# Performance work log

Measured on AMD Instinct MI355X. Metric: run time of the kernel, lower is better.

Reference implementation:

```python
import jax, jax.numpy as jnp
import numpy as np

LN_EPS = 1e-5

def _conv1d_same(x, w, b):
    # x: [B, L, Cin], w: [K, Cin, Cout] (kernel=3, padding=1 -> SAME)
    y = jax.lax.conv_general_dilated(x, w, window_strides=(1,), padding=[(1, 1)],
                                     dimension_numbers=('NWC', 'WIO', 'NWC'))
    return y + b

def _layer_norm(x, g, b):
    mu = jnp.mean(x, axis=-1, keepdims=True)
    var = jnp.var(x, axis=-1, keepdims=True)
    return (x - mu) * jax.lax.rsqrt(var + LN_EPS) * g + b

def _duration_predictor(x, conv1_w, conv1_b, ln1_g, ln1_b, conv2_w, conv2_b, ln2_g, ln2_b, lin_w, lin_b):
    h = jax.nn.relu(_layer_norm(_conv1d_same(x, conv1_w, conv1_b), ln1_g, ln1_b))
    h = jax.nn.relu(_layer_norm(_conv1d_same(h, conv2_w, conv2_b), ln2_g, ln2_b))
    out = jax.nn.relu(h @ lin_w + lin_b)  # [B, L, 1]
    return out[..., 0]  # squeeze -> [B, L]

def _length_regulate(x, dur, T):
    # Equivalent of alignment @ x without materializing [B, T, L] one-hot matrix.
    # Frame t copies phoneme j where cumsum(dur)[j-1] <= t < cumsum(dur)[j].
    ends = jnp.cumsum(dur, axis=-1)          # [B, L]
    total = ends[:, -1]                       # [B]
    t = jnp.arange(T)
    idx = jax.vmap(lambda e: jnp.searchsorted(e, t, side='right'))(ends)  # [B, T]
    idx = jnp.minimum(idx, dur.shape[1] - 1)
    gathered = jnp.take_along_axis(x, idx[:, :, None], axis=1)            # [B, T, D]
    mask = t[None, :] < total[:, None]                                    # [B, T]
    return jnp.where(mask[:, :, None], gathered, 0.0)

def setup_inputs() -> dict:
    key = jax.random.key(0)
    ks = jax.random.split(key, 8)
    B, L, D, F = 64, 512, 256, 256
    inp = {
        'x': jax.random.normal(ks[0], (B, L, D), dtype=jnp.float32),
        'target': jax.random.randint(ks[1], (B, L), 0, 8, dtype=jnp.int32),
        'mel_max_length': 4096,
        'conv1_w': jax.random.normal(ks[2], (3, D, F), dtype=jnp.float32) * 0.05,
        'conv1_b': jnp.zeros((F,), jnp.float32),
        'ln1_g': jnp.ones((F,), jnp.float32),
        'ln1_b': jnp.zeros((F,), jnp.float32),
        'conv2_w': jax.random.normal(ks[3], (3, F, F), dtype=jnp.float32) * 0.05,
        'conv2_b': jnp.zeros((F,), jnp.float32),
        'ln2_g': jnp.ones((F,), jnp.float32),
        'ln2_b': jnp.zeros((F,), jnp.float32),
        'lin_w': jax.random.normal(ks[4], (F, 1), dtype=jnp.float32) * 0.05,
        'lin_b': jnp.zeros((1,), jnp.float32),
    }
    return inp

def reference(x, target, mel_max_length, conv1_w, conv1_b, ln1_g, ln1_b, conv2_w, conv2_b, ln2_g, ln2_b, lin_w, lin_b):
    # Training path of LengthRegulator.forward (target given, dropout eval-mode identity)
    dp_out = _duration_predictor(x, conv1_w, conv1_b, ln1_g, ln1_b, conv2_w, conv2_b, ln2_g, ln2_b, lin_w, lin_b)
    output = _length_regulate(x, target, mel_max_length)  # padded to mel_max_length
    return output, dp_out
```

## Files before the change

kernel.cpp:

```cpp
#include <hip/hip_runtime.h>

#define B 64
#define L 512
#define D 256
#define T 4096
#define LN_EPS 1e-5f

typedef __attribute__((ext_vector_type(8))) short bf16x8;
typedef __attribute__((ext_vector_type(4))) float f32x4;

__device__ __forceinline__ unsigned short f2bf(float f) {
    unsigned int u = __float_as_uint(f);
    unsigned int r = (u + 0x7FFFu + ((u >> 16) & 1u)) >> 16;
    return (unsigned short)r;
}

__global__ __launch_bounds__(256) void cvt_w_kernel(const float* __restrict__ w1,
                                                    const float* __restrict__ w2,
                                                    unsigned short* __restrict__ o1,
                                                    unsigned short* __restrict__ o2) {
    const float* in = blockIdx.y ? w2 : w1;
    unsigned short* out = blockIdx.y ? o2 : o1;
    const int k = blockIdx.x;
    const int d0 = blockIdx.z * 32;
    const int f = threadIdx.x;
    for (int dc = 0; dc < 32; dc += 8) {
        unsigned short v[8];
#pragma unroll
        for (int i = 0; i < 8; ++i) v[i] = f2bf(in[(k * 256 + d0 + dc + i) * 256 + f]);
        *(bf16x8*)(out + (k * 256 + f) * 256 + d0 + dc) = *(bf16x8*)v;
    }
}

__global__ __launch_bounds__(64) void cumsum_kernel(const int* __restrict__ target,
                                                    int* __restrict__ ends) {
    int b = blockIdx.x;
    int lane = threadIdx.x;
    const int* trow = target + b * L;
    int* erow = ends + b * L;
    int vals[8];
    int base = lane * 8;
#pragma unroll
    for (int j = 0; j < 8; ++j) vals[j] = trow[base + j];
#pragma unroll
    for (int j = 1; j < 8; ++j) vals[j] += vals[j - 1];
    int lsum = vals[7];
    int s = lsum;
#pragma unroll
    for (int off = 1; off < 64; off <<= 1) {
        int v = __shfl_up(s, off, 64);
        if (lane >= off) s += v;
    }
    int excl = s - lsum;
#pragma unroll
    for (int j = 0; j < 8; ++j) erow[base + j] = excl + vals[j];
}

template <bool IN_F32, bool FUSE_LINEAR>
__global__ __launch_bounds__(256, 2) void conv_fused_kernel(
    const void* __restrict__ xin,
    const unsigned short* __restrict__ wT,
    const float* __restrict__ bias, const float* __restrict__ g, const float* __restrict__ beta,
    const float* __restrict__ lin_w, const float* __restrict__ lin_b,
    unsigned short* __restrict__ hout,
    float* __restrict__ dp)
{
    constexpr int LS = 264;
    __shared__ __align__(16) unsigned short xs[66 * LS];
    __shared__ float psum[64][2];
    __shared__ float psq[64][2];
    __shared__ float muA[64], rsA[64];

    const int tid = threadIdx.x;
    const int lane = tid & 63;
    const int wid = tid >> 6;
    const int l15 = lane & 15;
    const int g4 = lane >> 4;
    const int b = blockIdx.y;
    const int l0 = blockIdx.x * 64;
    const int wm = (wid >> 1) * 32;
    const int wn = (wid & 1) * 128;

    for (int i = tid; i < 66 * 32; i += 256) {
        int r = i >> 5, c = i & 31;
        int grow = l0 - 1 + r;
        bf16x8 v = {0, 0, 0, 0, 0, 0, 0, 0};
        if (grow >= 0 && grow < L) {
            if constexpr (IN_F32) {
                const float* xr = (const float*)xin + ((size_t)(b * L + grow)) * D + c * 8;
                float4 f0 = *(const float4*)xr;
                float4 f1 = *(const float4*)(xr + 4);
                unsigned short t[8] = {f2bf(f0.x), f2bf(f0.y), f2bf(f0.z), f2bf(f0.w),
                                       f2bf(f1.x), f2bf(f1.y), f2bf(f1.z), f2bf(f1.w)};
                v = *(bf16x8*)t;
            } else {
                v = *(const bf16x8*)((const unsigned short*)xin + ((size_t)(b * L + grow)) * D + c * 8);
            }
        }
        *(bf16x8*)(xs + r * LS + c * 8) = v;
    }
    __syncthreads();

    f32x4 acc[2][8];
#pragma unroll
    for (int m = 0; m < 2; ++m)
#pragma unroll
        for (int n = 0; n < 8; ++n) acc[m][n] = (f32x4){0.f, 0.f, 0.f, 0.f};

#pragma unroll 4
    for (int ks = 0; ks < 24; ++ks) {
        const int tap = ks >> 3, kk = ks & 7;
        const int r0 = wm + l15 + tap;
        bf16x8 a0 = *(const bf16x8*)(xs + r0 * LS + kk * 32 + g4 * 8);
        bf16x8 a1 = *(const bf16x8*)(xs + (r0 + 16) * LS + kk * 32 + g4 * 8);
        const unsigned short* wp = wT + tap * 65536 + (wn + l15) * 256 + kk * 32 + g4 * 8;
#pragma unroll
        for (int n = 0; n < 8; ++n) {
            bf16x8 bf = *(const bf16x8*)(wp + n * 4096);
            acc[0][n] = __builtin_amdgcn_mfma_f32_16x16x32_bf16(a0, bf, acc[0][n], 0, 0, 0);
            acc[1][n] = __builtin_amdgcn_mfma_f32_16x16x32_bf16(a1, bf, acc[1][n], 0, 0, 0);
        }
    }

    float biasv[8], gv[8], bv[8], lwv[8];
#pragma unroll
    for (int n = 0; n < 8; ++n) {
        int col = wn + n * 16 + l15;
        biasv[n] = bias[col];
        gv[n] = g[col];
        bv[n] = beta[col];
        lwv[n] = FUSE_LINEAR ? lin_w[col] : 0.f;
    }

#pragma unroll
    for (int m = 0; m < 2; ++m)
#pragma unroll
        for (int j = 0; j < 4; ++j) {
            float s = 0.f, q = 0.f;
#pragma unroll
            for (int n = 0; n < 8; ++n) {
                float v = acc[m][n][j] + biasv[n];
                s += v;
                q += v * v;
            }
#pragma unroll
            for (int off = 1; off < 16; off <<= 1) {
                s += __shfl_xor(s, off, 64);
                q += __shfl_xor(q, off, 64);
            }
            if (l15 == 0) {
                int row = wm + m * 16 + g4 * 4 + j;
                psum[row][wid & 1] = s;
                psq[row][wid & 1] = q;
            }
        }
    __syncthreads();
    if (tid < 64) {
        float s = psum[tid][0] + psum[tid][1];
        float q = psq[tid][0] + psq[tid][1];
        float mu = s * (1.f / 256.f);
        float var = q * (1.f / 256.f) - mu * mu;
        muA[tid] = mu;
        rsA[tid] = rsqrtf(var + LN_EPS);
    }
    __syncthreads();

    if constexpr (!FUSE_LINEAR) {
#pragma unroll
        for (int m = 0; m < 2; ++m)
#pragma unroll
            for (int j = 0; j < 4; ++j) {
                int row = wm + m * 16 + g4 * 4 + j;
                float mu = muA[row], rs = rsA[row];
                size_t base = ((size_t)(b * L + l0 + row)) * D + wn + l15;
#pragma unroll
                for (int n = 0; n < 8; ++n) {
                    float v = acc[m][n][j] + biasv[n];
                    float y = fmaxf((v - mu) * rs * gv[n] + bv[n], 0.f);
                    hout[base + n * 16] = f2bf(y);
                }
            }
    } else {
        float lb0 = lin_b[0];
#pragma unroll
        for (int m = 0; m < 2; ++m)
#pragma unroll
            for (int j = 0; j < 4; ++j) {
                int row = wm + m * 16 + g4 * 4 + j;
                float mu = muA[row], rs = rsA[row];
                float p = 0.f;
#pragma unroll
                for (int n = 0; n < 8; ++n) {
                    float v = acc[m][n][j] + biasv[n];
                    float y = fmaxf((v - mu) * rs * gv[n] + bv[n], 0.f);
                    p += y * lwv[n];
                }
#pragma unroll
                for (int off = 1; off < 16; off <<= 1) p += __shfl_xor(p, off, 64);
                if (l15 == 0) psum[row][wid & 1] = p;
            }
        __syncthreads();
        if (tid < 64) dp[b * L + l0 + tid] = fmaxf(psum[tid][0] + psum[tid][1] + lb0, 0.f);
    }
}

__global__ __launch_bounds__(256) void length_regulate_kernel(
    const float* __restrict__ x, const int* __restrict__ ends, float* __restrict__ out) {
    __shared__ int sidx[256];
    const int tid = threadIdx.x;
    const int lane = tid & 63;
    const int wid = tid >> 6;
    const int b = blockIdx.y;
    const int t0 = blockIdx.x * 256;
    const int* e = ends + b * L;
    const int total = e[L - 1];
    {
        int t = t0 + tid;
        int lo = 0, hi = L;
        while (lo < hi) {
            int mid = (lo + hi) >> 1;
            if (e[mid] <= t) lo = mid + 1; else hi = mid;
        }
        sidx[tid] = (lo < L - 1) ? lo : (L - 1);
    }
    __syncthreads();
    const float4* x4 = (const float4*)(x + (size_t)b * L * D);
    float4* o4 = (float4*)(out + (size_t)b * T * D);
    const float4 z = make_float4(0.f, 0.f, 0.f, 0.f);
#pragma unroll 4
    for (int rr = 0; rr < 64; ++rr) {
        int row = wid * 64 + rr;
        int t = t0 + row;
        float4 v = z;
        if (t < total) v = x4[sidx[row] * 64 + lane];
        o4[t * 64 + lane] = v;
    }
}

extern "C" void kernel_launch(void* const* d_in, const int* in_sizes, int n_in,
                              void* d_out, int out_size, void* d_ws, size_t ws_size,
                              hipStream_t stream) {
    const float* x   = (const float*)d_in[0];
    const int* target = (const int*)d_in[1];
    const float* c1w = (const float*)d_in[3];
    const float* c1b = (const float*)d_in[4];
    const float* g1  = (const float*)d_in[5];
    const float* b1  = (const float*)d_in[6];
    const float* c2w = (const float*)d_in[7];
    const float* c2b = (const float*)d_in[8];
    const float* g2  = (const float*)d_in[9];
    const float* b2  = (const float*)d_in[10];
    const float* lw  = (const float*)d_in[11];
    const float* lb  = (const float*)d_in[12];

    float* out = (float*)d_out;
    float* dp  = out + (size_t)B * T * D;

    char* base = (char*)d_out;
    unsigned short* h1  = (unsigned short*)(base);
    unsigned short* wT1 = (unsigned short*)(base + (32u << 20));
    unsigned short* wT2 = (unsigned short*)(base + (32u << 20) + 393216);
    int* ends = (int*)d_ws;

    cvt_w_kernel<<<dim3(3, 2, 8), dim3(256), 0, stream>>>(c1w, c2w, wT1, wT2);
    cumsum_kernel<<<dim3(B), dim3(64), 0, stream>>>(target, ends);
    conv_fused_kernel<true, false><<<dim3(L / 64, B), dim3(256), 0, stream>>>(
        x, wT1, c1b, g1, b1, nullptr, nullptr, h1, nullptr);
    conv_fused_kernel<false, true><<<dim3(L / 64, B), dim3(256), 0, stream>>>(
        h1, wT2, c2b, g2, b2, lw, lb, nullptr, dp);
    length_regulate_kernel<<<dim3(T / 256, B), dim3(256), 0, stream>>>(x, ends, out);
}
```

Baseline: 445.5 us.

## Merge prep kernels, halve conv row tile with weight prefetch, smem ends and nontemporal stores

The weight-conversion and cumsum kernels are merged into one launch. The conv kernel now uses 32-row tiles with one 16-row MFMA strip per wave, software-prefetches the next k-step's weight fragments into registers, and raises its occupancy hint to 3 blocks per CU. The length-regulate kernel stages the cumsum row in shared memory for its binary search and writes the large output with nontemporal stores. Smaller tiles double the number of conv blocks and halve reuse of each weight load per block, which raises global or L2 weight traffic.

```diff
diff --git a/kernel.cpp b/kernel.cpp
--- a/kernel.cpp
+++ b/kernel.cpp
@@ -15,49 +15,55 @@
     return (unsigned short)r;
 }
 
-__global__ __launch_bounds__(256) void cvt_w_kernel(const float* __restrict__ w1,
-                                                    const float* __restrict__ w2,
-                                                    unsigned short* __restrict__ o1,
-                                                    unsigned short* __restrict__ o2) {
-    const float* in = blockIdx.y ? w2 : w1;
-    unsigned short* out = blockIdx.y ? o2 : o1;
-    const int k = blockIdx.x;
-    const int d0 = blockIdx.z * 32;
-    const int f = threadIdx.x;
-    for (int dc = 0; dc < 32; dc += 8) {
-        unsigned short v[8];
-#pragma unroll
-        for (int i = 0; i < 8; ++i) v[i] = f2bf(in[(k * 256 + d0 + dc + i) * 256 + f]);
-        *(bf16x8*)(out + (k * 256 + f) * 256 + d0 + dc) = *(bf16x8*)v;
-    }
-}
-
-__global__ __launch_bounds__(64) void cumsum_kernel(const int* __restrict__ target,
-                                                    int* __restrict__ ends) {
-    int b = blockIdx.x;
-    int lane = threadIdx.x;
-    const int* trow = target + b * L;
-    int* erow = ends + b * L;
-    int vals[8];
-    int base = lane * 8;
-#pragma unroll
-    for (int j = 0; j < 8; ++j) vals[j] = trow[base + j];
-#pragma unroll
-    for (int j = 1; j < 8; ++j) vals[j] += vals[j - 1];
-    int lsum = vals[7];
-    int s = lsum;
-#pragma unroll
-    for (int off = 1; off < 64; off <<= 1) {
-        int v = __shfl_up(s, off, 64);
-        if (lane >= off) s += v;
-    }
-    int excl = s - lsum;
-#pragma unroll
-    for (int j = 0; j < 8; ++j) erow[base + j] = excl + vals[j];
+__global__ __launch_bounds__(256) void prep_kernel(const float* __restrict__ w1,
+                                                   const float* __restrict__ w2,
+                                                   unsigned short* __restrict__ o1,
+                                                   unsigned short* __restrict__ o2,
+                                                   const int* __restrict__ target,
+                                                   int* __restrict__ ends) {
+    const int bid = blockIdx.x;
+    const int tid = threadIdx.x;
+
+    if (tid < 64) {
+        const int lane = tid;
+        const int* trow = target + bid * L;
+        int* erow = ends + bid * L;
+        int vals[8];
+        int base = lane * 8;
+#pragma unroll
+        for (int j = 0; j < 8; ++j) vals[j] = trow[base + j];
+#pragma unroll
+        for (int j = 1; j < 8; ++j) vals[j] += vals[j - 1];
+        int lsum = vals[7];
+        int s = lsum;
+#pragma unroll
+        for (int off = 1; off < 64; off <<= 1) {
+            int v = __shfl_up(s, off, 64);
+            if (lane >= off) s += v;
+        }
+        int excl = s - lsum;
+#pragma unroll
+        for (int j = 0; j < 8; ++j) erow[base + j] = excl + vals[j];
+    }
+
+    if (bid < 48) {
+        const int k = bid % 3;
+        const int which = (bid / 3) & 1;
+        const int d0 = (bid / 6) * 32;
+        const float* in = which ? w2 : w1;
+        unsigned short* out = which ? o2 : o1;
+        const int f = tid;
+        for (int dc = 0; dc < 32; dc += 8) {
+            unsigned short v[8];
+#pragma unroll
+            for (int i = 0; i < 8; ++i) v[i] = f2bf(in[(k * 256 + d0 + dc + i) * 256 + f]);
+            *(bf16x8*)(out + (k * 256 + f) * 256 + d0 + dc) = *(bf16x8*)v;
+        }
+    }
 }
 
 template <bool IN_F32, bool FUSE_LINEAR>
-__global__ __launch_bounds__(256, 2) void conv_fused_kernel(
+__global__ __launch_bounds__(256, 3) void conv_fused_kernel(
     const void* __restrict__ xin,
     const unsigned short* __restrict__ wT,
     const float* __restrict__ bias, const float* __restrict__ g, const float* __restrict__ beta,
@@ -66,10 +72,10 @@
     float* __restrict__ dp)
 {
     constexpr int LS = 264;
-    __shared__ __align__(16) unsigned short xs[66 * LS];
-    __shared__ float psum[64][2];
-    __shared__ float psq[64][2];
-    __shared__ float muA[64], rsA[64];
+    __shared__ __align__(16) unsigned short xs[34 * LS];
+    __shared__ float psum[32][2];
+    __shared__ float psq[32][2];
+    __shared__ float muA[32], rsA[32];
 
     const int tid = threadIdx.x;
     const int lane = tid & 63;
@@ -77,19 +83,19 @@
     const int l15 = lane & 15;
     const int g4 = lane >> 4;
     const int b = blockIdx.y;
-    const int l0 = blockIdx.x * 64;
-    const int wm = (wid >> 1) * 32;
+    const int l0 = blockIdx.x * 32;
+    const int wr = wid >> 1;
     const int wn = (wid & 1) * 128;
 
-    for (int i = tid; i < 66 * 32; i += 256) {
+    for (int i = tid; i < 34 * 32; i += 256) {
         int r = i >> 5, c = i & 31;
         int grow = l0 - 1 + r;
         bf16x8 v = {0, 0, 0, 0, 0, 0, 0, 0};
         if (grow >= 0 && grow < L) {
             if constexpr (IN_F32) {
                 const float* xr = (const float*)xin + ((size_t)(b * L + grow)) * D + c * 8;
-                float4 f0 = *(const float4*)xr;
-                float4 f1 = *(const float4*)(xr + 4);
+                f32x4 f0 = *(const f32x4*)xr;
+                f32x4 f1 = *(const f32x4*)(xr + 4);
                 unsigned short t[8] = {f2bf(f0.x), f2bf(f0.y), f2bf(f0.z), f2bf(f0.w),
                                        f2bf(f1.x), f2bf(f1.y), f2bf(f1.z), f2bf(f1.w)};
                 v = *(bf16x8*)t;
@@ -101,25 +107,36 @@
     }
     __syncthreads();
 
-    f32x4 acc[2][8];
-#pragma unroll
-    for (int m = 0; m < 2; ++m)
-#pragma unroll
-        for (int n = 0; n < 8; ++n) acc[m][n] = (f32x4){0.f, 0.f, 0.f, 0.f};
+    f32x4 acc[8];
+#pragma unroll
+    for (int n = 0; n < 8; ++n) acc[n] = (f32x4){0.f, 0.f, 0.f, 0.f};
+
+    const unsigned short* wbase = wT + (wn + l15) * 256 + g4 * 8;
+
+    bf16x8 bcur[8];
+#pragma unroll
+    for (int n = 0; n < 8; ++n) bcur[n] = *(const bf16x8*)(wbase + n * 4096);
 
 #pragma unroll 4
-    for (int ks = 0; ks < 24; ++ks) {
+    for (int ks = 0; ks < 23; ++ks) {
         const int tap = ks >> 3, kk = ks & 7;
-        const int r0 = wm + l15 + tap;
-        bf16x8 a0 = *(const bf16x8*)(xs + r0 * LS + kk * 32 + g4 * 8);
-        bf16x8 a1 = *(const bf16x8*)(xs + (r0 + 16) * LS + kk * 32 + g4 * 8);
-        const unsigned short* wp = wT + tap * 65536 + (wn + l15) * 256 + kk * 32 + g4 * 8;
-#pragma unroll
-        for (int n = 0; n < 8; ++n) {
-            bf16x8 bf = *(const bf16x8*)(wp + n * 4096);
-            acc[0][n] = __builtin_amdgcn_mfma_f32_16x16x32_bf16(a0, bf, acc[0][n], 0, 0, 0);
-            acc[1][n] = __builtin_amdgcn_mfma_f32_16x16x32_bf16(a1, bf, acc[1][n], 0, 0, 0);
-        }
+        bf16x8 a0 = *(const bf16x8*)(xs + (wr * 16 + l15 + tap) * LS + kk * 32 + g4 * 8);
+        const int ksn = ks + 1;
+        const unsigned short* wp = wbase + (ksn >> 3) * 65536 + (ksn & 7) * 32;
+        bf16x8 bnext[8];
+#pragma unroll
+        for (int n = 0; n < 8; ++n) bnext[n] = *(const bf16x8*)(wp + n * 4096);
+#pragma unroll
+        for (int n = 0; n < 8; ++n)
+            acc[n] = __builtin_amdgcn_mfma_f32_16x16x32_bf16(a0, bcur[n], acc[n], 0, 0, 0);
+#pragma unroll
+        for (int n = 0; n < 8; ++n) bcur[n] = bnext[n];
+    }
+    {
+        bf16x8 a0 = *(const bf16x8*)(xs + (wr * 16 + l15 + 2) * LS + 7 * 32 + g4 * 8);
+#pragma unroll
+        for (int n = 0; n < 8; ++n)
+            acc[n] = __builtin_amdgcn_mfma_f32_16x16x32_bf16(a0, bcur[n], acc[n], 0, 0, 0);
     }
 
     float biasv[8], gv[8], bv[8], lwv[8];
@@ -133,29 +150,27 @@
     }
 
 #pragma unroll
-    for (int m = 0; m < 2; ++m)
-#pragma unroll
-        for (int j = 0; j < 4; ++j) {
-            float s = 0.f, q = 0.f;
-#pragma unroll
-            for (int n = 0; n < 8; ++n) {
-                float v = acc[m][n][j] + biasv[n];
-                s += v;
-                q += v * v;
-            }
-#pragma unroll
-            for (int off = 1; off < 16; off <<= 1) {
-                s += __shfl_xor(s, off, 64);
-                q += __shfl_xor(q, off, 64);
-            }
-            if (l15 == 0) {
-                int row = wm + m * 16 + g4 * 4 + j;
-                psum[row][wid & 1] = s;
-                psq[row][wid & 1] = q;
-            }
-        }
-    __syncthreads();
-    if (tid < 64) {
+    for (int j = 0; j < 4; ++j) {
+        float s = 0.f, q = 0.f;
+#pragma unroll
+        for (int n = 0; n < 8; ++n) {
+            float v = acc[n][j] + biasv[n];
+            s += v;
+            q += v * v;
+        }
+#pragma unroll
+        for (int off = 1; off < 16; off <<= 1) {
+            s += __shfl_xor(s, off, 64);
+            q += __shfl_xor(q, off, 64);
+        }
+        if (l15 == 0) {
+            int row = wr * 16 + g4 * 4 + j;
+            psum[row][wid & 1] = s;
+            psq[row][wid & 1] = q;
+        }
+    }
+    __syncthreads();
+    if (tid < 32) {
         float s = psum[tid][0] + psum[tid][1];
         float q = psq[tid][0] + psq[tid][1];
         float mu = s * (1.f / 256.f);
@@ -167,45 +182,42 @@
 
     if constexpr (!FUSE_LINEAR) {
 #pragma unroll
-        for (int m = 0; m < 2; ++m)
-#pragma unroll
-            for (int j = 0; j < 4; ++j) {
-                int row = wm + m * 16 + g4 * 4 + j;
-                float mu = muA[row], rs = rsA[row];
-                size_t base = ((size_t)(b * L + l0 + row)) * D + wn + l15;
-#pragma unroll
-                for (int n = 0; n < 8; ++n) {
-                    float v = acc[m][n][j] + biasv[n];
-                    float y = fmaxf((v - mu) * rs * gv[n] + bv[n], 0.f);
-                    hout[base + n * 16] = f2bf(y);
-                }
+        for (int j = 0; j < 4; ++j) {
+            int row = wr * 16 + g4 * 4 + j;
+            float mu = muA[row], rs = rsA[row];
+            size_t base = ((size_t)(b * L + l0 + row)) * D + wn + l15;
+#pragma unroll
+            for (int n = 0; n < 8; ++n) {
+                float v = acc[n][j] + biasv[n];
+                float y = fmaxf((v - mu) * rs * gv[n] + bv[n], 0.f);
+                hout[base + n * 16] = f2bf(y);
             }
+        }
     } else {
         float lb0 = lin_b[0];
 #pragma unroll
-        for (int m = 0; m < 2; ++m)
-#pragma unroll
-            for (int j = 0; j < 4; ++j) {
-                int row = wm + m * 16 + g4 * 4 + j;
-                float mu = muA[row], rs = rsA[row];
-                float p = 0.f;
-#pragma unroll
-                for (int n = 0; n < 8; ++n) {
-                    float v = acc[m][n][j] + biasv[n];
-                    float y = fmaxf((v - mu) * rs * gv[n] + bv[n], 0.f);
-                    p += y * lwv[n];
-                }
-#pragma unroll
-                for (int off = 1; off < 16; off <<= 1) p += __shfl_xor(p, off, 64);
-                if (l15 == 0) psum[row][wid & 1] = p;
+        for (int j = 0; j < 4; ++j) {
+            int row = wr * 16 + g4 * 4 + j;
+            float mu = muA[row], rs = rsA[row];
+            float p = 0.f;
+#pragma unroll
+            for (int n = 0; n < 8; ++n) {
+                float v = acc[n][j] + biasv[n];
+                float y = fmaxf((v - mu) * rs * gv[n] + bv[n], 0.f);
+                p += y * lwv[n];
             }
+#pragma unroll
+            for (int off = 1; off < 16; off <<= 1) p += __shfl_xor(p, off, 64);
+            if (l15 == 0) psum[row][wid & 1] = p;
+        }
         __syncthreads();
-        if (tid < 64) dp[b * L + l0 + tid] = fmaxf(psum[tid][0] + psum[tid][1] + lb0, 0.f);
+        if (tid < 32) dp[b * L + l0 + tid] = fmaxf(psum[tid][0] + psum[tid][1] + lb0, 0.f);
     }
 }
 
 __global__ __launch_bounds__(256) void length_regulate_kernel(
     const float* __restrict__ x, const int* __restrict__ ends, float* __restrict__ out) {
+    __shared__ int se[512];
     __shared__ int sidx[256];
     const int tid = threadIdx.x;
     const int lane = tid & 63;
@@ -213,27 +225,30 @@
     const int b = blockIdx.y;
     const int t0 = blockIdx.x * 256;
     const int* e = ends + b * L;
-    const int total = e[L - 1];
+    se[tid] = e[tid];
+    se[tid + 256] = e[tid + 256];
+    __syncthreads();
+    const int total = se[511];
     {
         int t = t0 + tid;
         int lo = 0, hi = L;
         while (lo < hi) {
             int mid = (lo + hi) >> 1;
-            if (e[mid] <= t) lo = mid + 1; else hi = mid;
+            if (se[mid] <= t) lo = mid + 1; else hi = mid;
         }
         sidx[tid] = (lo < L - 1) ? lo : (L - 1);
     }
     __syncthreads();
-    const float4* x4 = (const float4*)(x + (size_t)b * L * D);
-    float4* o4 = (float4*)(out + (size_t)b * T * D);
-    const float4 z = make_float4(0.f, 0.f, 0.f, 0.f);
+    const f32x4* x4 = (const f32x4*)(x + (size_t)b * L * D);
+    f32x4* o4 = (f32x4*)(out + (size_t)b * T * D);
+    const f32x4 z = (f32x4){0.f, 0.f, 0.f, 0.f};
 #pragma unroll 4
     for (int rr = 0; rr < 64; ++rr) {
         int row = wid * 64 + rr;
         int t = t0 + row;
-        float4 v = z;
+        f32x4 v = z;
         if (t < total) v = x4[sidx[row] * 64 + lane];
-        o4[t * 64 + lane] = v;
+        __builtin_nontemporal_store(v, &o4[(size_t)t * 64 + lane]);
     }
 }
 
@@ -262,11 +277,10 @@
     unsigned short* wT2 = (unsigned short*)(base + (32u << 20) + 393216);
     int* ends = (int*)d_ws;
 
-    cvt_w_kernel<<<dim3(3, 2, 8), dim3(256), 0, stream>>>(c1w, c2w, wT1, wT2);
-    cumsum_kernel<<<dim3(B), dim3(64), 0, stream>>>(target, ends);
-    conv_fused_kernel<true, false><<<dim3(L / 64, B), dim3(256), 0, stream>>>(
+    prep_kernel<<<dim3(64), dim3(256), 0, stream>>>(c1w, c2w, wT1, wT2, target, ends);
+    conv_fused_kernel<true, false><<<dim3(L / 32, B), dim3(256), 0, stream>>>(
         x, wT1, c1b, g1, b1, nullptr, nullptr, h1, nullptr);
-    conv_fused_kernel<false, true><<<dim3(L / 64, B), dim3(256), 0, stream>>>(
+    conv_fused_kernel<false, true><<<dim3(L / 32, B), dim3(256), 0, stream>>>(
         h1, wT2, c2b, g2, b2, lw, lb, nullptr, dp);
     length_regulate_kernel<<<dim3(T / 256, B), dim3(256), 0, stream>>>(x, ends, out);
 }
```

Result: slower. 502.2 us (+12.7%).
